# Optimization experiments

Hardware: AMD Instinct MI355X
Metric: run time of the kernel (lower is better)

The kernel has to match this reference:

```python
import jax, jax.numpy as jnp
import numpy as np

V, F, N = 5143, 10144, 2_000_000


def _safe_normalize(x):
    # matches GaussianAvatars safe_normalize: x / sqrt(clamp(|x|^2, min=1e-20))
    return x * jax.lax.rsqrt(jnp.clip(jnp.sum(x * x, axis=-1, keepdims=True), 1e-20, None))


def _quat_wxyz_to_rotmat(q):
    # rotation_activation (L2 normalize with eps) then wxyz->xyzw + roma unitquat_to_rotmat
    q = q / (jnp.sqrt(jnp.sum(q * q, axis=-1, keepdims=True)) + 1e-12)
    w, x, y, z = q[..., 0], q[..., 1], q[..., 2], q[..., 3]
    R = jnp.stack([
        jnp.stack([1 - 2 * (y * y + z * z), 2 * (x * y - z * w), 2 * (x * z + y * w)], axis=-1),
        jnp.stack([2 * (x * y + z * w), 1 - 2 * (x * x + z * z), 2 * (y * z - x * w)], axis=-1),
        jnp.stack([2 * (x * z - y * w), 2 * (y * z + x * w), 1 - 2 * (x * x + y * y)], axis=-1),
    ], axis=-2)
    return R  # [N,3,3]


def setup_inputs() -> dict:
    key = jax.random.key(0)
    ks = jax.random.split(key, 9)
    verts = jax.random.normal(ks[0], (V, 3), jnp.float32) * 0.1
    faces = jax.random.randint(ks[1], (F, 3), 0, V, dtype=jnp.int32)
    binding = jax.random.randint(ks[2], (N,), 0, F, dtype=jnp.int32)
    xyz = jax.random.normal(ks[3], (N, 3), jnp.float32) * 0.01
    rotation = jax.random.normal(ks[4], (N, 4), jnp.float32)
    scaling = jax.random.normal(ks[5], (N, 3), jnp.float32) - 4.0
    opacity = jax.random.normal(ks[6], (N, 1), jnp.float32)
    features_dc = jax.random.normal(ks[7], (N, 1, 3), jnp.float32)
    features_rest = jax.random.normal(ks[8], (N, 15, 3), jnp.float32) * 0.1
    return dict(verts=verts, faces=faces, binding=binding, xyz=xyz, rotation=rotation,
                scaling=scaling, opacity=opacity, features_dc=features_dc,
                features_rest=features_rest)


def reference(verts, faces, binding, xyz, rotation, scaling, opacity, features_dc, features_rest):
    # --- per-face geometry (compute_face_orientation + face_center) ---
    v0 = verts[faces[:, 0]]  # [F,3]
    v1 = verts[faces[:, 1]]
    v2 = verts[faces[:, 2]]
    face_center = (v0 + v1 + v2) / 3.0  # triangles.mean(dim=-2)
    e01 = v1 - v0
    e02 = v2 - v0
    a0 = _safe_normalize(e01)
    a1 = _safe_normalize(jnp.cross(a0, e02))
    a2 = -_safe_normalize(jnp.cross(a1, a0))
    face_orien_mat = jnp.stack([a0, a1, a2], axis=-1)  # [F,3,3], columns = axes
    s0 = jnp.sqrt(jnp.sum(e01 * e01, axis=-1, keepdims=True))
    s1 = jnp.abs(jnp.sum(a2 * e02, axis=-1, keepdims=True))
    face_scaling = 0.5 * (s0 + s1)  # [F,1]

    # --- binding-indexed gathers ---
    O_b = face_orien_mat[binding]      # [N,3,3]
    fs_b = face_scaling[binding]       # [N,1]
    fc_b = face_center[binding]        # [N,3]

    # --- gaussian position in world space ---
    xyz_out = jnp.einsum('nij,nj->ni', O_b, xyz) * fs_b + fc_b  # [N,3]

    # --- color (dc sh band 0 + opacity), scaled to 0..255 ---
    op = jax.nn.sigmoid(opacity)  # [N,1]
    color = jnp.clip((jnp.concatenate([0.5 + 0.282 * features_dc[:, 0, :], op], axis=-1)) * 255.0, 0.0, 255.0)

    # --- covariance build ---
    scales = jnp.exp(scaling) * fs_b  # [N,3]
    Q = _quat_wxyz_to_rotmat(rotation)  # [N,3,3]
    rotations = jnp.swapaxes(jnp.einsum('nij,njk->nik', O_b, Q), 1, 2)  # (O@Q)^T, [N,3,3]
    sig = rotations * scales[:, :, None]  # einsum('bij,bi->bij')
    C = jnp.einsum('nij,nik->njk', sig, sig)  # [N,3,3] = sig^T sig
    simga = jnp.stack([C[:, 0, 0], C[:, 0, 1], C[:, 0, 2], C[:, 1, 1], C[:, 1, 2], C[:, 2, 2]], axis=-1)

    return jnp.concatenate([xyz_out, color, simga], axis=-1)  # [N,13]
```

## Files before the change

kernel.cpp:

```cpp
#include <hip/hip_runtime.h>
#include <math.h>

typedef float f4 __attribute__((ext_vector_type(4)));
typedef float f2 __attribute__((ext_vector_type(2)));
typedef _Float16 h8 __attribute__((ext_vector_type(8)));

struct F3 { float x, y, z; };

__device__ __forceinline__ F3 f3(float x, float y, float z) { return {x, y, z}; }
__device__ __forceinline__ F3 add(F3 a, F3 b) { return {a.x+b.x, a.y+b.y, a.z+b.z}; }
__device__ __forceinline__ F3 sub(F3 a, F3 b) { return {a.x-b.x, a.y-b.y, a.z-b.z}; }
__device__ __forceinline__ F3 mul(F3 a, float s) { return {a.x*s, a.y*s, a.z*s}; }
__device__ __forceinline__ float dot3(F3 a, F3 b) { return a.x*b.x + a.y*b.y + a.z*b.z; }
__device__ __forceinline__ F3 cross3(F3 a, F3 b) {
    return {a.y*b.z - a.z*b.y, a.z*b.x - a.x*b.z, a.x*b.y - a.y*b.x};
}
__device__ __forceinline__ F3 safe_normalize(F3 a) {
    float d = dot3(a, a);
    float inv = rsqrtf(fmaxf(d, 1e-20f));
    return mul(a, inv);
}

#define BLK 256

__global__ __launch_bounds__(BLK) void face_precompute_kernel(
    const float* __restrict__ verts, const int* __restrict__ faces,
    h8* __restrict__ tab, int F)
{
    const int f = blockIdx.x * BLK + threadIdx.x;
    if (f >= F) return;
    const int f0 = faces[3*f+0], f1 = faces[3*f+1], f2 = faces[3*f+2];
    const F3 v0 = f3(verts[3*f0], verts[3*f0+1], verts[3*f0+2]);
    const F3 v1 = f3(verts[3*f1], verts[3*f1+1], verts[3*f1+2]);
    const F3 v2 = f3(verts[3*f2], verts[3*f2+1], verts[3*f2+2]);

    const F3 fc  = mul(add(add(v0, v1), v2), (1.0f/3.0f));
    const F3 e01 = sub(v1, v0);
    const F3 e02 = sub(v2, v0);
    const F3 a0 = safe_normalize(e01);
    const F3 a1 = safe_normalize(cross3(a0, e02));
    const F3 a2 = mul(safe_normalize(cross3(a1, a0)), -1.0f);
    const float s0 = sqrtf(dot3(e01, e01));
    const float s1 = fabsf(dot3(a2, e02));
    const float fs = 0.5f * (s0 + s1);

    const float R00 = a0.x, R10 = a0.y, R20 = a0.z;
    const float R01 = a1.x, R11 = a1.y, R21 = a1.z;
    const float R02 = a2.x, R12 = a2.y, R22 = a2.z;
    float qw, qx, qy, qz;
    const float tr = R00 + R11 + R22;
    if (tr > 0.0f) {
        const float s = 0.5f / sqrtf(tr + 1.0f);
        qw = 0.25f / s;
        qx = (R21 - R12) * s;
        qy = (R02 - R20) * s;
        qz = (R10 - R01) * s;
    } else if (R00 > R11 && R00 > R22) {
        const float s = 2.0f * sqrtf(1.0f + R00 - R11 - R22);
        qw = (R21 - R12) / s;
        qx = 0.25f * s;
        qy = (R01 + R10) / s;
        qz = (R02 + R20) / s;
    } else if (R11 > R22) {
        const float s = 2.0f * sqrtf(1.0f + R11 - R00 - R22);
        qw = (R02 - R20) / s;
        qx = (R01 + R10) / s;
        qy = 0.25f * s;
        qz = (R12 + R21) / s;
    } else {
        const float s = 2.0f * sqrtf(1.0f + R22 - R00 - R11);
        qw = (R10 - R01) / s;
        qx = (R02 + R20) / s;
        qy = (R12 + R21) / s;
        qz = 0.25f * s;
    }
    const float qn = rsqrtf(fmaxf(qw*qw + qx*qx + qy*qy + qz*qz, 1e-30f));
    qw *= qn; qx *= qn; qy *= qn; qz *= qn;

    h8 rec;
    rec[0] = (_Float16)fc.x; rec[1] = (_Float16)fc.y;
    rec[2] = (_Float16)fc.z; rec[3] = (_Float16)fs;
    rec[4] = (_Float16)qw;   rec[5] = (_Float16)qx;
    rec[6] = (_Float16)qy;   rec[7] = (_Float16)qz;
    tab[f] = rec;
}

struct Out13 {
    float o0,o1,o2,o3,o4,o5,o6,o7,o8,o9,o10,o11,o12;
};

__device__ __forceinline__ Out13 compute_point(
    float px, float py, float pz,
    float rw, float rx, float ry, float rz,
    float sc0, float sc1, float sc2,
    float opa, float d0, float d1, float d2,
    h8 rec)
{
    const float fcx = (float)rec[0], fcy = (float)rec[1], fcz = (float)rec[2];
    const float fs  = (float)rec[3];
    const float fw  = (float)rec[4], fx = (float)rec[5];
    const float fy  = (float)rec[6], fz = (float)rec[7];

    const float ttx = 2.0f*(fy*pz - fz*py);
    const float tty = 2.0f*(fz*px - fx*pz);
    const float ttz = 2.0f*(fx*py - fy*px);
    const float vx = px + fw*ttx + (fy*ttz - fz*tty);
    const float vy = py + fw*tty + (fz*ttx - fx*ttz);
    const float vz = pz + fw*ttz + (fx*tty - fy*ttx);

    const float qd = rw*rw + rx*rx + ry*ry + rz*rz;
    const float qi = rsqrtf(fmaxf(qd, 1e-24f));
    const float pw = rw*qi, pxq = rx*qi, pyq = ry*qi, pzq = rz*qi;

    const float tw = fw*pw  - fx*pxq - fy*pyq - fz*pzq;
    const float tx = fw*pxq + fx*pw  + fy*pzq - fz*pyq;
    const float ty = fw*pyq - fx*pzq + fy*pw  + fz*pxq;
    const float tz = fw*pzq + fx*pyq - fy*pxq + fz*pw;

    const float m0x = 1.0f - 2.0f*(ty*ty + tz*tz);
    const float m0y = 2.0f*(tx*ty + tz*tw);
    const float m0z = 2.0f*(tx*tz - ty*tw);
    const float m1x = 2.0f*(tx*ty - tz*tw);
    const float m1y = 1.0f - 2.0f*(tx*tx + tz*tz);
    const float m1z = 2.0f*(ty*tz + tx*tw);
    const float m2x = 2.0f*(tx*tz + ty*tw);
    const float m2y = 2.0f*(ty*tz - tx*tw);
    const float m2z = 1.0f - 2.0f*(tx*tx + ty*ty);

    const float w0 = __expf(sc0) * fs;
    const float w1 = __expf(sc1) * fs;
    const float w2 = __expf(sc2) * fs;
    const float t0s = w0*w0, t1s = w1*w1, t2s = w2*w2;

    Out13 o;
    o.o0 = vx*fs + fcx;
    o.o1 = vy*fs + fcy;
    o.o2 = vz*fs + fcz;
    o.o3 = fminf(fmaxf((0.5f + 0.282f*d0) * 255.0f, 0.0f), 255.0f);
    o.o4 = fminf(fmaxf((0.5f + 0.282f*d1) * 255.0f, 0.0f), 255.0f);
    o.o5 = fminf(fmaxf((0.5f + 0.282f*d2) * 255.0f, 0.0f), 255.0f);
    const float sg = 1.0f / (1.0f + __expf(-opa));
    o.o6 = fminf(fmaxf(sg * 255.0f, 0.0f), 255.0f);
    o.o7  = t0s*m0x*m0x + t1s*m1x*m1x + t2s*m2x*m2x;
    o.o8  = t0s*m0x*m0y + t1s*m1x*m1y + t2s*m2x*m2y;
    o.o9  = t0s*m0x*m0z + t1s*m1x*m1z + t2s*m2x*m2z;
    o.o10 = t0s*m0y*m0y + t1s*m1y*m1y + t2s*m2y*m2y;
    o.o11 = t0s*m0y*m0z + t1s*m1y*m1z + t2s*m2y*m2z;
    o.o12 = t0s*m0z*m0z + t1s*m1z*m1z + t2s*m2z*m2z;
    return o;
}

__device__ __forceinline__ void store13(float* s, const Out13& o) {
    s[0] = o.o0;  s[1] = o.o1;  s[2]  = o.o2;  s[3]  = o.o3;
    s[4] = o.o4;  s[5] = o.o5;  s[6]  = o.o6;  s[7]  = o.o7;
    s[8] = o.o8;  s[9] = o.o9;  s[10] = o.o10; s[11] = o.o11; s[12] = o.o12;
}

__global__ __launch_bounds__(BLK) void gauss_main2_kernel(
    const h8*    __restrict__ tab,
    const int*   __restrict__ binding,
    const float* __restrict__ xyz,
    const float* __restrict__ rot,
    const float* __restrict__ scal,
    const float* __restrict__ opac,
    const float* __restrict__ fdc,
    float*       __restrict__ out,
    int N)
{
    __shared__ __align__(16) float sout[2 * BLK * 13];

    const int tid   = threadIdx.x;
    const int t     = blockIdx.x * BLK + tid;
    const int pbase = blockIdx.x * (BLK * 2);
    const int p0    = 2 * t;
    const int count = min(2 * BLK, N - pbase);

    if (p0 + 1 < N) {
        const int2 b2 = reinterpret_cast<const int2*>(binding)[t];
        const f2 xa = reinterpret_cast<const f2*>(xyz )[3*t    ];
        const f2 xb = reinterpret_cast<const f2*>(xyz )[3*t + 1];
        const f2 xc = reinterpret_cast<const f2*>(xyz )[3*t + 2];
        const f2 sa = reinterpret_cast<const f2*>(scal)[3*t    ];
        const f2 sb = reinterpret_cast<const f2*>(scal)[3*t + 1];
        const f2 scv= reinterpret_cast<const f2*>(scal)[3*t + 2];
        const f2 da = reinterpret_cast<const f2*>(fdc )[3*t    ];
        const f2 db = reinterpret_cast<const f2*>(fdc )[3*t + 1];
        const f2 dc = reinterpret_cast<const f2*>(fdc )[3*t + 2];
        const f4 qA = reinterpret_cast<const f4*>(rot )[2*t    ];
        const f4 qB = reinterpret_cast<const f4*>(rot )[2*t + 1];
        const f2 op2 = reinterpret_cast<const f2*>(opac)[t];
        const h8 recA = tab[b2.x];
        const h8 recB = tab[b2.y];

        const Out13 A = compute_point(xa.x, xa.y, xb.x,
                                      qA.x, qA.y, qA.z, qA.w,
                                      sa.x, sa.y, sb.x,
                                      op2.x, da.x, da.y, db.x, recA);
        const Out13 B = compute_point(xb.y, xc.x, xc.y,
                                      qB.x, qB.y, qB.z, qB.w,
                                      sb.y, scv.x, scv.y,
                                      op2.y, db.y, dc.x, dc.y, recB);

        store13(sout + (size_t)(2*tid    ) * 13, A);
        store13(sout + (size_t)(2*tid + 1) * 13, B);
    } else {
        for (int p = p0; p < N; ++p) {
            const int b = binding[p];
            const h8 rec = tab[b];
            const Out13 o = compute_point(
                xyz[3*p], xyz[3*p+1], xyz[3*p+2],
                rot[4*p], rot[4*p+1], rot[4*p+2], rot[4*p+3],
                scal[3*p], scal[3*p+1], scal[3*p+2],
                opac[p], fdc[3*p], fdc[3*p+1], fdc[3*p+2], rec);
            store13(sout + (size_t)(p - pbase) * 13, o);
        }
    }

    __syncthreads();

    const int total = count * 13;
    const size_t obase = (size_t)pbase * 13;
    const int n4 = total >> 2;
    const f4* sf = reinterpret_cast<const f4*>(sout);
    f4* o4 = reinterpret_cast<f4*>(out + obase);
    for (int j = tid; j < n4; j += BLK) o4[j] = sf[j];
    for (int j = (n4 << 2) + tid; j < total; j += BLK) out[obase + j] = sout[j];
}

__global__ __launch_bounds__(BLK) void gauss_fused_kernel(
    const float* __restrict__ verts, const int* __restrict__ faces,
    const int* __restrict__ binding, const float* __restrict__ xyz,
    const float* __restrict__ rot, const float* __restrict__ scal,
    const float* __restrict__ opac, const float* __restrict__ fdc,
    float* __restrict__ out, int N)
{
    const int i = blockIdx.x * BLK + threadIdx.x;
    if (i >= N) return;
    const int b = binding[i];
    const int f0 = faces[3*b+0], f1 = faces[3*b+1], f2 = faces[3*b+2];
    const F3 v0 = f3(verts[3*f0], verts[3*f0+1], verts[3*f0+2]);
    const F3 v1 = f3(verts[3*f1], verts[3*f1+1], verts[3*f1+2]);
    const F3 v2 = f3(verts[3*f2], verts[3*f2+1], verts[3*f2+2]);
    const F3 fc  = mul(add(add(v0, v1), v2), (1.0f/3.0f));
    const F3 e01 = sub(v1, v0);
    const F3 e02 = sub(v2, v0);
    const F3 a0 = safe_normalize(e01);
    const F3 a1 = safe_normalize(cross3(a0, e02));
    const float s0 = sqrtf(dot3(e01, e01));
    const F3 a2 = mul(safe_normalize(cross3(a1, a0)), -1.0f);
    const float s1 = fabsf(dot3(a2, e02));
    const float fs = 0.5f * (s0 + s1);

    const float px = xyz[3*i], py = xyz[3*i+1], pz = xyz[3*i+2];
    const float qw0 = rot[4*i], qx0 = rot[4*i+1], qy0 = rot[4*i+2], qz0 = rot[4*i+3];
    const float sc0 = scal[3*i], sc1 = scal[3*i+1], sc2 = scal[3*i+2];
    const float opa = opac[i];
    const float d0 = fdc[3*i], d1 = fdc[3*i+1], d2 = fdc[3*i+2];

    F3 xo = add(add(mul(a0, px), mul(a1, py)), mul(a2, pz));
    xo = add(mul(xo, fs), fc);

    const float qn = sqrtf(qw0*qw0 + qx0*qx0 + qy0*qy0 + qz0*qz0) + 1e-12f;
    const float qi = 1.0f / qn;
    const float w = qw0*qi, x = qx0*qi, y = qy0*qi, z = qz0*qi;
    const float Q00 = 1.0f - 2.0f*(y*y + z*z);
    const float Q01 = 2.0f*(x*y - z*w);
    const float Q02 = 2.0f*(x*z + y*w);
    const float Q10 = 2.0f*(x*y + z*w);
    const float Q11 = 1.0f - 2.0f*(x*x + z*z);
    const float Q12 = 2.0f*(y*z - x*w);
    const float Q20 = 2.0f*(x*z - y*w);
    const float Q21 = 2.0f*(y*z + x*w);
    const float Q22 = 1.0f - 2.0f*(x*x + y*y);

    const F3 m0 = add(add(mul(a0, Q00), mul(a1, Q10)), mul(a2, Q20));
    const F3 m1 = add(add(mul(a0, Q01), mul(a1, Q11)), mul(a2, Q21));
    const F3 m2 = add(add(mul(a0, Q02), mul(a1, Q12)), mul(a2, Q22));

    const float w0 = __expf(sc0) * fs;
    const float w1 = __expf(sc1) * fs;
    const float w2 = __expf(sc2) * fs;
    const float t0s = w0*w0, t1s = w1*w1, t2s = w2*w2;

    float* op = out + (size_t)i * 13;
    op[0] = xo.x; op[1] = xo.y; op[2] = xo.z;
    op[3] = fminf(fmaxf((0.5f + 0.282f*d0) * 255.0f, 0.0f), 255.0f);
    op[4] = fminf(fmaxf((0.5f + 0.282f*d1) * 255.0f, 0.0f), 255.0f);
    op[5] = fminf(fmaxf((0.5f + 0.282f*d2) * 255.0f, 0.0f), 255.0f);
    op[6] = fminf(fmaxf((1.0f/(1.0f+__expf(-opa))) * 255.0f, 0.0f), 255.0f);
    op[7]  = t0s*m0.x*m0.x + t1s*m1.x*m1.x + t2s*m2.x*m2.x;
    op[8]  = t0s*m0.x*m0.y + t1s*m1.x*m1.y + t2s*m2.x*m2.y;
    op[9]  = t0s*m0.x*m0.z + t1s*m1.x*m1.z + t2s*m2.x*m2.z;
    op[10] = t0s*m0.y*m0.y + t1s*m1.y*m1.y + t2s*m2.y*m2.y;
    op[11] = t0s*m0.y*m0.z + t1s*m1.y*m1.z + t2s*m2.y*m2.z;
    op[12] = t0s*m0.z*m0.z + t1s*m1.z*m1.z + t2s*m2.z*m2.z;
}

extern "C" void kernel_launch(void* const* d_in, const int* in_sizes, int n_in,
                              void* d_out, int out_size, void* d_ws, size_t ws_size,
                              hipStream_t stream) {
    const float* verts   = (const float*)d_in[0];
    const int*   faces   = (const int*)  d_in[1];
    const int*   binding = (const int*)  d_in[2];
    const float* xyz     = (const float*)d_in[3];
    const float* rot     = (const float*)d_in[4];
    const float* scal    = (const float*)d_in[5];
    const float* opac    = (const float*)d_in[6];
    const float* fdc     = (const float*)d_in[7];
    float* out = (float*)d_out;
    const int N = in_sizes[2];
    const int F = in_sizes[1] / 3;

    const size_t tab_bytes = (size_t)F * sizeof(h8);

    if (ws_size >= tab_bytes) {
        h8* tab = (h8*)d_ws;
        const int fblocks = (F + BLK - 1) / BLK;
        face_precompute_kernel<<<fblocks, BLK, 0, stream>>>(verts, faces, tab, F);
        const int NT = (N + 1) / 2;
        const int blocks = (NT + BLK - 1) / BLK;
        gauss_main2_kernel<<<blocks, BLK, 0, stream>>>(
            tab, binding, xyz, rot, scal, opac, fdc, out, N);
    } else {
        const int blocks = (N + BLK - 1) / BLK;
        gauss_fused_kernel<<<blocks, BLK, 0, stream>>>(
            verts, faces, binding, xyz, rot, scal, opac, fdc, out, N);
    }
}
```

Baseline: 43.91 us.

## Process four points per thread and store outputs directly as float4

Each thread now handles four gaussians instead of two, so every per-point input stream can be loaded with 16-byte vector loads. The four 13-float outputs (52 floats) are written straight to global memory as thirteen float4 stores, which removes the shared-memory staging buffer and the block-wide barrier. The cost is more registers per thread and half as many threads. Each thread's stores are contiguous but strided across lanes, which may reduce coalescing compared with the staged copy.

```diff
diff --git a/kernel.cpp b/kernel.cpp
--- a/kernel.cpp
+++ b/kernel.cpp
@@ -2,7 +2,6 @@
 #include <math.h>
 
 typedef float f4 __attribute__((ext_vector_type(4)));
-typedef float f2 __attribute__((ext_vector_type(2)));
 typedef _Float16 h8 __attribute__((ext_vector_type(8)));
 
 struct F3 { float x, y, z; };
@@ -150,13 +149,11 @@
     return o;
 }
 
-__device__ __forceinline__ void store13(float* s, const Out13& o) {
-    s[0] = o.o0;  s[1] = o.o1;  s[2]  = o.o2;  s[3]  = o.o3;
-    s[4] = o.o4;  s[5] = o.o5;  s[6]  = o.o6;  s[7]  = o.o7;
-    s[8] = o.o8;  s[9] = o.o9;  s[10] = o.o10; s[11] = o.o11; s[12] = o.o12;
-}
-
-__global__ __launch_bounds__(BLK) void gauss_main2_kernel(
+__device__ __forceinline__ f4 mkf4(float a, float b, float c, float d) {
+    f4 v; v.x = a; v.y = b; v.z = c; v.w = d; return v;
+}
+
+__global__ __launch_bounds__(BLK) void gauss_main4_kernel(
     const h8*    __restrict__ tab,
     const int*   __restrict__ binding,
     const float* __restrict__ xyz,
@@ -167,42 +164,63 @@
     float*       __restrict__ out,
     int N)
 {
-    __shared__ __align__(16) float sout[2 * BLK * 13];
-
-    const int tid   = threadIdx.x;
-    const int t     = blockIdx.x * BLK + tid;
-    const int pbase = blockIdx.x * (BLK * 2);
-    const int p0    = 2 * t;
-    const int count = min(2 * BLK, N - pbase);
-
-    if (p0 + 1 < N) {
-        const int2 b2 = reinterpret_cast<const int2*>(binding)[t];
-        const f2 xa = reinterpret_cast<const f2*>(xyz )[3*t    ];
-        const f2 xb = reinterpret_cast<const f2*>(xyz )[3*t + 1];
-        const f2 xc = reinterpret_cast<const f2*>(xyz )[3*t + 2];
-        const f2 sa = reinterpret_cast<const f2*>(scal)[3*t    ];
-        const f2 sb = reinterpret_cast<const f2*>(scal)[3*t + 1];
-        const f2 scv= reinterpret_cast<const f2*>(scal)[3*t + 2];
-        const f2 da = reinterpret_cast<const f2*>(fdc )[3*t    ];
-        const f2 db = reinterpret_cast<const f2*>(fdc )[3*t + 1];
-        const f2 dc = reinterpret_cast<const f2*>(fdc )[3*t + 2];
-        const f4 qA = reinterpret_cast<const f4*>(rot )[2*t    ];
-        const f4 qB = reinterpret_cast<const f4*>(rot )[2*t + 1];
-        const f2 op2 = reinterpret_cast<const f2*>(opac)[t];
-        const h8 recA = tab[b2.x];
-        const h8 recB = tab[b2.y];
-
-        const Out13 A = compute_point(xa.x, xa.y, xb.x,
+    const int t  = blockIdx.x * BLK + threadIdx.x;
+    const int NT = (N + 3) >> 2;
+    if (t >= NT) return;
+    const int p0 = 4 * t;
+
+    if (p0 + 3 < N) {
+        const int4 b4 = reinterpret_cast<const int4*>(binding)[t];
+        const f4 xa = reinterpret_cast<const f4*>(xyz)[3*t    ];
+        const f4 xb = reinterpret_cast<const f4*>(xyz)[3*t + 1];
+        const f4 xc = reinterpret_cast<const f4*>(xyz)[3*t + 2];
+        const f4 sa = reinterpret_cast<const f4*>(scal)[3*t    ];
+        const f4 sb = reinterpret_cast<const f4*>(scal)[3*t + 1];
+        const f4 sc = reinterpret_cast<const f4*>(scal)[3*t + 2];
+        const f4 da = reinterpret_cast<const f4*>(fdc)[3*t    ];
+        const f4 db = reinterpret_cast<const f4*>(fdc)[3*t + 1];
+        const f4 dc = reinterpret_cast<const f4*>(fdc)[3*t + 2];
+        const f4 qA = reinterpret_cast<const f4*>(rot)[4*t    ];
+        const f4 qB = reinterpret_cast<const f4*>(rot)[4*t + 1];
+        const f4 qC = reinterpret_cast<const f4*>(rot)[4*t + 2];
+        const f4 qD = reinterpret_cast<const f4*>(rot)[4*t + 3];
+        const f4 op4 = reinterpret_cast<const f4*>(opac)[t];
+        const h8 recA = tab[b4.x];
+        const h8 recB = tab[b4.y];
+        const h8 recC = tab[b4.z];
+        const h8 recD = tab[b4.w];
+
+        const Out13 A = compute_point(xa.x, xa.y, xa.z,
                                       qA.x, qA.y, qA.z, qA.w,
-                                      sa.x, sa.y, sb.x,
-                                      op2.x, da.x, da.y, db.x, recA);
-        const Out13 B = compute_point(xb.y, xc.x, xc.y,
+                                      sa.x, sa.y, sa.z,
+                                      op4.x, da.x, da.y, da.z, recA);
+        const Out13 B = compute_point(xa.w, xb.x, xb.y,
                                       qB.x, qB.y, qB.z, qB.w,
-                                      sb.y, scv.x, scv.y,
-                                      op2.y, db.y, dc.x, dc.y, recB);
-
-        store13(sout + (size_t)(2*tid    ) * 13, A);
-        store13(sout + (size_t)(2*tid + 1) * 13, B);
+                                      sa.w, sb.x, sb.y,
+                                      op4.y, da.w, db.x, db.y, recB);
+        const Out13 C = compute_point(xb.z, xb.w, xc.x,
+                                      qC.x, qC.y, qC.z, qC.w,
+                                      sb.z, sb.w, sc.x,
+                                      op4.z, db.z, db.w, dc.x, recC);
+        const Out13 D = compute_point(xc.y, xc.z, xc.w,
+                                      qD.x, qD.y, qD.z, qD.w,
+                                      sc.y, sc.z, sc.w,
+                                      op4.w, dc.y, dc.z, dc.w, recD);
+
+        f4* o4 = reinterpret_cast<f4*>(out + (size_t)t * 52);
+        o4[0]  = mkf4(A.o0,  A.o1,  A.o2,  A.o3);
+        o4[1]  = mkf4(A.o4,  A.o5,  A.o6,  A.o7);
+        o4[2]  = mkf4(A.o8,  A.o9,  A.o10, A.o11);
+        o4[3]  = mkf4(A.o12, B.o0,  B.o1,  B.o2);
+        o4[4]  = mkf4(B.o3,  B.o4,  B.o5,  B.o6);
+        o4[5]  = mkf4(B.o7,  B.o8,  B.o9,  B.o10);
+        o4[6]  = mkf4(B.o11, B.o12, C.o0,  C.o1);
+        o4[7]  = mkf4(C.o2,  C.o3,  C.o4,  C.o5);
+        o4[8]  = mkf4(C.o6,  C.o7,  C.o8,  C.o9);
+        o4[9]  = mkf4(C.o10, C.o11, C.o12, D.o0);
+        o4[10] = mkf4(D.o1,  D.o2,  D.o3,  D.o4);
+        o4[11] = mkf4(D.o5,  D.o6,  D.o7,  D.o8);
+        o4[12] = mkf4(D.o9,  D.o10, D.o11, D.o12);
     } else {
         for (int p = p0; p < N; ++p) {
             const int b = binding[p];
@@ -212,19 +230,13 @@
                 rot[4*p], rot[4*p+1], rot[4*p+2], rot[4*p+3],
                 scal[3*p], scal[3*p+1], scal[3*p+2],
                 opac[p], fdc[3*p], fdc[3*p+1], fdc[3*p+2], rec);
-            store13(sout + (size_t)(p - pbase) * 13, o);
+            float* op = out + (size_t)p * 13;
+            op[0] = o.o0;  op[1] = o.o1;  op[2]  = o.o2;  op[3]  = o.o3;
+            op[4] = o.o4;  op[5] = o.o5;  op[6]  = o.o6;  op[7]  = o.o7;
+            op[8] = o.o8;  op[9] = o.o9;  op[10] = o.o10; op[11] = o.o11;
+            op[12] = o.o12;
         }
     }
-
-    __syncthreads();
-
-    const int total = count * 13;
-    const size_t obase = (size_t)pbase * 13;
-    const int n4 = total >> 2;
-    const f4* sf = reinterpret_cast<const f4*>(sout);
-    f4* o4 = reinterpret_cast<f4*>(out + obase);
-    for (int j = tid; j < n4; j += BLK) o4[j] = sf[j];
-    for (int j = (n4 << 2) + tid; j < total; j += BLK) out[obase + j] = sout[j];
 }
 
 __global__ __launch_bounds__(BLK) void gauss_fused_kernel(
@@ -317,9 +329,9 @@
         h8* tab = (h8*)d_ws;
         const int fblocks = (F + BLK - 1) / BLK;
         face_precompute_kernel<<<fblocks, BLK, 0, stream>>>(verts, faces, tab, F);
-        const int NT = (N + 1) / 2;
+        const int NT = (N + 3) / 4;
         const int blocks = (NT + BLK - 1) / BLK;
-        gauss_main2_kernel<<<blocks, BLK, 0, stream>>>(
+        gauss_main4_kernel<<<blocks, BLK, 0, stream>>>(
             tab, binding, xyz, rot, scal, opac, fdc, out, N);
     } else {
         const int blocks = (N + BLK - 1) / BLK;
```

Result: slower. 63.72 us (+45.1%).
